# Performance work log

Measured on AMD Instinct MI355X. Metric: run time of the kernel, lower is better.

## Reference

```python
import jax, jax.numpy as jnp
import numpy as np
import math

D = 1024      # d_model
K = 64        # k_eigenstates
H = 4         # n_heads
KH = K // H   # eigenstates per head
MLP = 4 * D
B, T = 4, 4096


def setup_inputs() -> dict:
    key = jax.random.key(0)
    ks = jax.random.split(key, 16)
    rn = lambda k, shape, s: (jax.random.normal(k, shape, jnp.float32) * s)
    inp = {
        "x": rn(ks[0], (B, T, D), 1.0),
        "W_in": rn(ks[1], (2 * K, D), 1.0 / math.sqrt(D)),
        "log_decay": jax.random.uniform(ks[2], (K,), jnp.float32, -3.0, -0.1),
        "frequency": jnp.linspace(0.0, 2 * math.pi * (1 - 1.0 / K), K, dtype=jnp.float32),
        "W_sel": rn(ks[3], (2 * K, D), 0.01 / math.sqrt(D)),
        "b_sel": jnp.zeros((2 * K,), jnp.float32),
        "R": jnp.eye(KH, dtype=jnp.float32)[None] + 0.01 * rn(ks[4], (H, KH, KH), 1.0 / math.sqrt(KH)),
        "W_out": rn(ks[5], (D, 2 * K), 1.0 / math.sqrt(2 * K)),
        "W_g": rn(ks[6], (D, D), 1.0 / math.sqrt(D)),
        "b_g": jnp.full((D,), -2.0, jnp.float32),
        "g1": jnp.ones((D,), jnp.float32),
        "be1": jnp.zeros((D,), jnp.float32),
        "g2": jnp.ones((D,), jnp.float32),
        "be2": jnp.zeros((D,), jnp.float32),
        "W1": rn(ks[7], (MLP, D), 1.0 / math.sqrt(D)),
        "b1": jnp.zeros((MLP,), jnp.float32),
        "W2": rn(ks[8], (D, MLP), 1.0 / math.sqrt(MLP)),
        "b2": jnp.zeros((D,), jnp.float32),
    }
    return inp


def _ln(x, g, b):
    m = jnp.mean(x, axis=-1, keepdims=True)
    v = jnp.mean(jnp.square(x - m), axis=-1, keepdims=True)
    return (x - m) * jax.lax.rsqrt(v + 1e-5) * g + b


def _scan_combine(e1, e2):
    a1, b1 = e1
    a2, b2 = e2
    return a1 * a2, a2 * b1 + b2


def reference(x, W_in, log_decay, frequency, W_sel, b_sel, R, W_out, W_g, b_g,
              g1, be1, g2, be2, W1, b1, W2, b2):
    Bsz, Ts, Dm = x.shape
    residual = x
    x_norm = _ln(x, g1, be1)

    beta = x_norm @ W_in.T                      # [B,T,2K]
    beta_r, beta_i = jnp.split(beta, 2, axis=-1)

    delta = x_norm @ W_sel.T + b_sel            # selective modulation
    d_dec, d_fr = jnp.split(delta, 2, axis=-1)
    mag = jax.nn.sigmoid(log_decay + 0.1 * jnp.tanh(d_dec))   # [B,T,K]
    freq = frequency + 0.05 * jnp.tanh(d_fr)

    a = jax.lax.complex(mag * jnp.cos(freq), mag * jnp.sin(freq))  # lambda_t
    bc = jax.lax.complex(beta_r, beta_i)
    # inclusive prefix scan of c_t = a_t * c_{t-1} + b_t
    _, c = jax.lax.associative_scan(_scan_combine, (a, bc), axis=1)
    c_r, c_i = c.real, c.imag                   # [B,T,K]

    nH, Kh = R.shape[0], R.shape[1]
    c_r = jnp.einsum('hjk,bthk->bthj', R, c_r.reshape(Bsz, Ts, nH, Kh)).reshape(Bsz, Ts, -1)
    c_i = jnp.einsum('hjk,bthk->bthj', R, c_i.reshape(Bsz, Ts, nH, Kh)).reshape(Bsz, Ts, -1)

    h = jnp.concatenate([c_r, c_i], axis=-1) @ W_out.T
    gate = jax.nn.sigmoid(x_norm @ W_g.T + b_g)
    x = residual + gate * h

    x2 = _ln(x, g2, be2)
    x = x + (jax.nn.silu(x2 @ W1.T + b1) @ W2.T + b2)
    return x
```

## Files before the change

kernel.cpp:

```cpp
#include <hip/hip_runtime.h>
#include <math.h>

typedef __bf16 bf16_t;
typedef __attribute__((ext_vector_type(8))) __bf16 bf16x8;
typedef __attribute__((ext_vector_type(4))) float f32x4;

#define DMODEL 1024
#define NROWS  16384
#define SEQLEN 4096

static __device__ __forceinline__ float sigmoidf_(float v) { return 1.f / (1.f + __expf(-v)); }

#define GLOAD16(gsrc, ldst) __builtin_amdgcn_global_load_lds(                     \
    (const __attribute__((address_space(1))) void*)(gsrc),                        \
    (__attribute__((address_space(3))) void*)(ldst), 16, 0, 0)

__global__ __launch_bounds__(256) void ln_fused_kernel(const float* __restrict__ x,
                                                       const float* __restrict__ g,
                                                       const float* __restrict__ b,
                                                       bf16_t* __restrict__ out) {
  int row = blockIdx.x;
  int tid = threadIdx.x;
  const float4* xr = (const float4*)(x + (size_t)row * DMODEL);
  float4 v = xr[tid];
  float s  = v.x + v.y + v.z + v.w;
  float s2 = v.x*v.x + v.y*v.y + v.z*v.z + v.w*v.w;
  #pragma unroll
  for (int off = 32; off > 0; off >>= 1) {
    s  += __shfl_down(s, off);
    s2 += __shfl_down(s2, off);
  }
  __shared__ float sh[4], sh2[4];
  int lane = tid & 63, wid = tid >> 6;
  if (lane == 0) { sh[wid] = s; sh2[wid] = s2; }
  __syncthreads();
  s  = sh[0] + sh[1] + sh[2] + sh[3];
  s2 = sh2[0] + sh2[1] + sh2[2] + sh2[3];
  float m = s * (1.f / DMODEL);
  float var = fmaxf(s2 * (1.f / DMODEL) - m * m, 0.f);
  float rs = rsqrtf(var + 1e-5f);
  float4 gv = *(const float4*)&g[tid * 4];
  float4 bv = *(const float4*)&b[tid * 4];
  union { bf16_t h[4]; float2 f2; } u;
  u.h[0] = (bf16_t)((v.x - m) * rs * gv.x + bv.x);
  u.h[1] = (bf16_t)((v.y - m) * rs * gv.y + bv.y);
  u.h[2] = (bf16_t)((v.z - m) * rs * gv.z + bv.z);
  u.h[3] = (bf16_t)((v.w - m) * rs * gv.w + bv.w);
  *(float2*)&out[(size_t)row * DMODEL + tid * 4] = u.f2;
}

__global__ __launch_bounds__(256) void f32_to_bf16_kernel(const float* __restrict__ in,
                                                          bf16_t* __restrict__ out, int n) {
  int idx = (blockIdx.x * 256 + threadIdx.x) * 4;
  if (idx >= n) return;
  float4 v = *(const float4*)&in[idx];
  union { bf16_t h[4]; float2 f2; } u;
  u.h[0] = (bf16_t)v.x; u.h[1] = (bf16_t)v.y; u.h[2] = (bf16_t)v.z; u.h[3] = (bf16_t)v.w;
  *(float2*)&out[idx] = u.f2;
}

#define LOADA(d, mh)                                                              \
  { _Pragma("unroll")                                                             \
    for (int m_ = 0; m_ < 4; ++m_) {                                              \
      _Pragma("unroll")                                                           \
      for (int kk_ = 0; kk_ < 2; ++kk_)                                           \
        afrag[m_][kk_] = *(const bf16x8*)(ldsp + (d) * 32768 + (mh) * 16384 +     \
            (aRow + m_ * 16) * 128 + ((kk_ * 64 + q16) ^ swz));                   \
    } }

#define LOADB(d, nn)                                                              \
  { _Pragma("unroll")                                                             \
    for (int n2_ = 0; n2_ < 2; ++n2_) {                                           \
      _Pragma("unroll")                                                           \
      for (int kk_ = 0; kk_ < 2; ++kk_)                                           \
        bfrag[nn][n2_][kk_] = *(const bf16x8*)(ldsp + 65536 + (d) * 32768 +       \
            (nn) * 16384 + (bRow + n2_ * 16) * 128 + ((kk_ * 64 + q16) ^ swz));   \
    } }

#define MFMAQ(mh, nn)                                                             \
  { _Pragma("unroll")                                                             \
    for (int m_ = 0; m_ < 4; ++m_) {                                              \
      _Pragma("unroll")                                                           \
      for (int n2_ = 0; n2_ < 2; ++n2_) {                                         \
        acc[(mh)*4+m_][(nn)*2+n2_] = __builtin_amdgcn_mfma_f32_16x16x32_bf16(     \
            afrag[m_][0], bfrag[nn][n2_][0], acc[(mh)*4+m_][(nn)*2+n2_], 0,0,0);  \
        acc[(mh)*4+m_][(nn)*2+n2_] = __builtin_amdgcn_mfma_f32_16x16x32_bf16(     \
            afrag[m_][1], bfrag[nn][n2_][1], acc[(mh)*4+m_][(nn)*2+n2_], 0,0,0);  \
      }                                                                           \
    } }

#define PH_PRE()  __builtin_amdgcn_s_barrier();                                   \
                  asm volatile("s_waitcnt lgkmcnt(0)");                           \
                  __builtin_amdgcn_sched_barrier(0);                              \
                  __builtin_amdgcn_s_setprio(1)
#define PH_POST() __builtin_amdgcn_s_setprio(0);                                  \
                  __builtin_amdgcn_s_barrier()

template<int EPI>
__global__ __launch_bounds__(512, 2) void gemm256_kernel(
    const bf16_t* __restrict__ A, int lda,
    const bf16_t* __restrict__ B, int ldb, int K, int nx,
    const float* __restrict__ bias,
    const float* __restrict__ res,
    const float* __restrict__ aux,
    float* __restrict__ outf, bf16_t* __restrict__ outb, int ldout) {
  __shared__ __align__(128) char ldsp[131072];
  const int nwg = gridDim.x;
  const int bid = blockIdx.x;
  const int lid = (bid & 7) * (nwg >> 3) + (bid >> 3);
  const int n0 = (lid % nx) * 256;
  const int r0 = (lid / nx) * 256;

  const int tid = threadIdx.x;
  const int lane = tid & 63;
  const int w = tid >> 6;
  const int wr = w >> 2, wc = w & 3;
  const int fr = lane & 15;
  const int q16 = (lane >> 4) * 16;
  const int swz = (fr & 7) << 4;
  const int aRow = wr * 64 + fr;
  const int bRow = wc * 32 + fr;

  const size_t lda_b = (size_t)lda * 2;
  const size_t ldb_b = (size_t)ldb * 2;
  const char* Ab = (const char*)A;
  const char* Bb = (const char*)B;
  const int trow = tid >> 3;
  const int scolb = (((tid & 7) ^ (trow & 7)) << 4);

  auto stageA = [&](int d, int h, int kt) {
    const char* src = Ab + (size_t)(r0 + h * 64 + trow) * lda_b + kt * 128 + scolb;
    char* dst = ldsp + d * 32768 + h * 16384 + tid * 16;
    GLOAD16(src, dst);
    GLOAD16(src + 128 * lda_b, dst + 8192);
  };
  auto stageB = [&](int d, int g, int kt) {
    const int r1 = 64 + trow;
    const char* s0 = Bb + (size_t)(n0 + (trow >> 5) * 64 + g * 32 + (trow & 31)) * ldb_b + kt * 128 + scolb;
    const char* s1 = Bb + (size_t)(n0 + (r1 >> 5) * 64 + g * 32 + (r1 & 31)) * ldb_b + kt * 128 + scolb;
    char* dst = ldsp + 65536 + d * 32768 + g * 16384 + tid * 16;
    GLOAD16(s0, dst);
    GLOAD16(s1, dst + 8192);
  };

  f32x4 acc[8][4];
  #pragma unroll
  for (int m = 0; m < 8; ++m)
    #pragma unroll
    for (int n = 0; n < 4; ++n) acc[m][n] = (f32x4){0.f, 0.f, 0.f, 0.f};
  bf16x8 afrag[4][2];
  bf16x8 bfrag[2][2][2];

  const int nt = K >> 6;

  stageA(0, 0, 0); stageB(0, 0, 0); stageB(0, 1, 0); stageA(0, 1, 0);
  if (nt > 1) {
    stageA(1, 0, 1); stageB(1, 0, 1); stageB(1, 1, 1);
    asm volatile("s_waitcnt vmcnt(6)");
  } else {
    asm volatile("s_waitcnt vmcnt(0)");
  }
  __builtin_amdgcn_s_barrier();

  for (int t = 0; t < nt - 1; ++t) {
    const int d = t & 1, dn = d ^ 1;
    LOADA(d, 0) LOADB(d, 0)
    stageA(dn, 1, t + 1);
    PH_PRE(); MFMAQ(0, 0) PH_POST();
    LOADB(d, 1)
    if (t + 2 < nt) stageA(d, 0, t + 2);
    PH_PRE(); MFMAQ(0, 1) PH_POST();
    LOADA(d, 1)
    if (t + 2 < nt) stageB(d, 0, t + 2);
    PH_PRE(); MFMAQ(1, 0) PH_POST();
    if (t + 2 < nt) stageB(d, 1, t + 2);
    __builtin_amdgcn_s_barrier();
    __builtin_amdgcn_s_setprio(1);
    MFMAQ(1, 1)
    __builtin_amdgcn_s_setprio(0);
    if (t == nt - 2) { asm volatile("s_waitcnt vmcnt(0)"); }
    else             { asm volatile("s_waitcnt vmcnt(6)"); }
    __builtin_amdgcn_s_barrier();
  }
  {
    const int d = (nt - 1) & 1;
    LOADA(d, 0) LOADB(d, 0)
    asm volatile("s_waitcnt lgkmcnt(0)");
    __builtin_amdgcn_sched_barrier(0);
    MFMAQ(0, 0)
    LOADB(d, 1)
    asm volatile("s_waitcnt lgkmcnt(0)");
    __builtin_amdgcn_sched_barrier(0);
    MFMAQ(0, 1)
    LOADA(d, 1)
    asm volatile("s_waitcnt lgkmcnt(0)");
    __builtin_amdgcn_sched_barrier(0);
    MFMAQ(1, 0)
    MFMAQ(1, 1)
  }

  const int rbase = (lane >> 4) * 4;
  #pragma unroll
  for (int mf = 0; mf < 8; ++mf) {
    #pragma unroll
    for (int n = 0; n < 4; ++n) {
      int row = r0 + wr * 128 + mf * 16 + rbase;
      int col = n0 + wc * 64 + n * 16 + fr;
      f32x4 v = acc[mf][n];
      #pragma unroll
      for (int j = 0; j < 4; ++j) {
        int r = row + j;
        float val = v[j];
        if (EPI == 0) {
          outf[(size_t)r * ldout + col] = val;
        } else if (EPI == 1) {
          float t2 = val + bias[col];
          t2 = t2 * sigmoidf_(t2);
          outb[(size_t)r * ldout + col] = (bf16_t)t2;
        } else if (EPI == 2) {
          outf[(size_t)r * ldout + col] = res[(size_t)r * 1024 + col] + bias[col] + val;
        } else if (EPI == 3) {
          outf[(size_t)r * ldout + col] += val;
        } else {
          size_t idx = (size_t)r * 1024 + col;
          outf[idx] = res[idx] + sigmoidf_(val + bias[col]) * aux[idx];
        }
      }
    }
  }
}

template<int EPI>
__global__ __launch_bounds__(256) void gemm_bf16_kernel(
    const bf16_t* __restrict__ A, int lda,
    const bf16_t* __restrict__ B, int ldb, int K, int nx,
    float* __restrict__ outf, int ldout) {
  __shared__ __align__(16) bf16_t As[128 * 32];
  __shared__ __align__(16) bf16_t Bs[128 * 32];
  const int nwg = gridDim.x;
  const int bid = blockIdx.x;
  const int lid = (bid & 7) * (nwg >> 3) + (bid >> 3);
  const int n0 = (lid % nx) * 128;
  const int r0 = (lid / nx) * 128;

  const int tid = threadIdx.x;
  const int lane = tid & 63;
  const int w = tid >> 6;
  const int wr = w >> 1, wc = w & 1;
  const int srow0 = tid >> 2;
  const int srow1 = 64 + (tid >> 2);
  const int skk = (tid & 3) * 8;
  const int fr = lane & 15;
  const int ko = (lane >> 4) * 8;

  f32x4 acc[4][4];
  #pragma unroll
  for (int m = 0; m < 4; ++m)
    #pragma unroll
    for (int n = 0; n < 4; ++n) acc[m][n] = (f32x4){0.f, 0.f, 0.f, 0.f};

  for (int k0 = 0; k0 < K; k0 += 32) {
    GLOAD16(A + (size_t)(r0 + srow0) * lda + k0 + skk, (char*)As + w * 1024);
    GLOAD16(A + (size_t)(r0 + srow1) * lda + k0 + skk, (char*)As + 4096 + w * 1024);
    GLOAD16(B + (size_t)(n0 + srow0) * ldb + k0 + skk, (char*)Bs + w * 1024);
    GLOAD16(B + (size_t)(n0 + srow1) * ldb + k0 + skk, (char*)Bs + 4096 + w * 1024);
    __syncthreads();
    bf16x8 af[4], bfr[4];
    #pragma unroll
    for (int m = 0; m < 4; ++m)
      af[m] = *(const bf16x8*)&As[(wr * 64 + m * 16 + fr) * 32 + ko];
    #pragma unroll
    for (int n = 0; n < 4; ++n)
      bfr[n] = *(const bf16x8*)&Bs[(wc * 64 + n * 16 + fr) * 32 + ko];
    #pragma unroll
    for (int m = 0; m < 4; ++m)
      #pragma unroll
      for (int n = 0; n < 4; ++n)
        acc[m][n] = __builtin_amdgcn_mfma_f32_16x16x32_bf16(af[m], bfr[n], acc[m][n], 0, 0, 0);
    __syncthreads();
  }

  const int rbase = (lane >> 4) * 4;
  #pragma unroll
  for (int m = 0; m < 4; ++m) {
    #pragma unroll
    for (int n = 0; n < 4; ++n) {
      int row = r0 + wr * 64 + m * 16 + rbase;
      int col = n0 + wc * 64 + n * 16 + fr;
      f32x4 v = acc[m][n];
      #pragma unroll
      for (int j = 0; j < 4; ++j)
        outf[(size_t)(row + j) * ldout + col] = v[j];
    }
  }
}

__global__ __launch_bounds__(256) void ew_ab_kernel(
    const float* __restrict__ bd, const float* __restrict__ b_sel,
    const float* __restrict__ log_decay, const float* __restrict__ frequency,
    float* __restrict__ a_r, float* __restrict__ a_i,
    float* __restrict__ b_r, float* __restrict__ b_i) {
  __shared__ float T[32][257];
  int bb = blockIdx.x >> 7;
  int t0 = (blockIdx.x & 127) << 5;
  int tid = threadIdx.x;
  #pragma unroll
  for (int p = 0; p < 32; ++p) {
    int idx = tid + p * 256;
    int tt = idx >> 8, j = idx & 255;
    T[tt][j] = bd[((size_t)bb * 4096 + t0 + tt) * 256 + j];
  }
  __syncthreads();
  #pragma unroll
  for (int p = 0; p < 8; ++p) {
    int idx = tid + p * 256;
    int tt = idx & 31, k = idx >> 5;
    float br_ = T[tt][k];
    float bi_ = T[tt][64 + k];
    float dd = T[tt][128 + k] + b_sel[k];
    float df = T[tt][192 + k] + b_sel[64 + k];
    float mag = sigmoidf_(log_decay[k] + 0.1f * tanhf(dd));
    float fr = frequency[k] + 0.05f * tanhf(df);
    float ar_ = mag * cosf(fr), ai_ = mag * sinf(fr);
    size_t o = ((size_t)bb * 64 + k) * 4096 + t0 + tt;
    a_r[o] = ar_; a_i[o] = ai_; b_r[o] = br_; b_i[o] = bi_;
  }
}

__global__ __launch_bounds__(256) void scan_kernel(
    const float* __restrict__ a_r, const float* __restrict__ a_i,
    const float* b_r, const float* b_i,
    float* c_r, float* c_i) {
  int seq = blockIdx.x;
  size_t base = (size_t)seq * SEQLEN;
  int tid = threadIdx.x;
  int t0 = tid * 16;
  float Ar = 1.f, Ai = 0.f, Br = 0.f, Bi = 0.f;
  #pragma unroll
  for (int s = 0; s < 16; ++s) {
    size_t t = base + t0 + s;
    float ar = a_r[t], ai = a_i[t], br = b_r[t], bi = b_i[t];
    float nBr = ar * Br - ai * Bi + br;
    float nBi = ar * Bi + ai * Br + bi;
    Br = nBr; Bi = nBi;
    float nAr = ar * Ar - ai * Ai;
    float nAi = ar * Ai + ai * Ar;
    Ar = nAr; Ai = nAi;
  }
  __shared__ float sAr[256], sAi[256], sBr[256], sBi[256];
  sAr[tid] = Ar; sAi[tid] = Ai; sBr[tid] = Br; sBi[tid] = Bi;
  for (int off = 1; off < 256; off <<= 1) {
    __syncthreads();
    float pAr = 0.f, pAi = 0.f, pBr = 0.f, pBi = 0.f;
    if (tid >= off) { pAr = sAr[tid - off]; pAi = sAi[tid - off]; pBr = sBr[tid - off]; pBi = sBi[tid - off]; }
    __syncthreads();
    if (tid >= off) {
      float cAr = sAr[tid], cAi = sAi[tid], cBr = sBr[tid], cBi = sBi[tid];
      float nBr = cAr * pBr - cAi * pBi + cBr;
      float nBi = cAr * pBi + cAi * pBr + cBi;
      float nAr = cAr * pAr - cAi * pAi;
      float nAi = cAr * pAi + cAi * pAr;
      sAr[tid] = nAr; sAi[tid] = nAi; sBr[tid] = nBr; sBi[tid] = nBi;
    }
  }
  __syncthreads();
  float cr = (tid > 0) ? sBr[tid - 1] : 0.f;
  float ci = (tid > 0) ? sBi[tid - 1] : 0.f;
  #pragma unroll
  for (int s = 0; s < 16; ++s) {
    size_t t = base + t0 + s;
    float ar = a_r[t], ai = a_i[t], br = b_r[t], bi = b_i[t];
    float nr = ar * cr - ai * ci + br;
    float ni = ar * ci + ai * cr + bi;
    cr = nr; ci = ni;
    c_r[t] = cr; c_i[t] = ci;
  }
}

__global__ __launch_bounds__(256) void transpose_cc_kernel(
    const float* __restrict__ c_r, const float* __restrict__ c_i,
    bf16_t* __restrict__ cc) {
  __shared__ float Tr[64][65];
  __shared__ float Ti[64][65];
  int t0 = blockIdx.x * 64;
  int bb = blockIdx.y;
  int tid = threadIdx.x;
  int tt = tid & 63;
  int q = tid >> 6;
  #pragma unroll
  for (int p = 0; p < 16; ++p) {
    int k = p * 4 + q;
    size_t src = ((size_t)bb * 64 + k) * 4096 + t0 + tt;
    Tr[tt][k] = c_r[src];
    Ti[tt][k] = c_i[src];
  }
  __syncthreads();
  #pragma unroll
  for (int p = 0; p < 16; ++p) {
    int tt2 = p * 4 + q;
    int k = tid & 63;
    size_t row = (size_t)bb * 4096 + t0 + tt2;
    cc[row * 128 + k] = (bf16_t)Tr[tt2][k];
    cc[row * 128 + 64 + k] = (bf16_t)Ti[tt2][k];
  }
}

__global__ __launch_bounds__(256) void weff_kernel(const float* __restrict__ W_out,
                                                   const float* __restrict__ R,
                                                   bf16_t* __restrict__ Weff) {
  int idx = blockIdx.x * 256 + threadIdx.x;
  int d = idx >> 7, col = idx & 127;
  int k = col & 63, h = k >> 4, kk = k & 15;
  int off = (col < 64) ? 0 : 64;
  float s = 0.f;
  #pragma unroll
  for (int j = 0; j < 16; ++j)
    s += W_out[d * 128 + off + h * 16 + j] * R[h * 256 + j * 16 + kk];
  Weff[idx] = (bf16_t)s;
}

extern "C" void kernel_launch(void* const* d_in, const int* in_sizes, int n_in,
                              void* d_out, int out_size, void* d_ws, size_t ws_size,
                              hipStream_t stream) {
  (void)in_sizes; (void)n_in; (void)out_size; (void)ws_size;
  const float* x         = (const float*)d_in[0];
  const float* W_in      = (const float*)d_in[1];
  const float* log_decay = (const float*)d_in[2];
  const float* frequency = (const float*)d_in[3];
  const float* W_sel     = (const float*)d_in[4];
  const float* b_sel     = (const float*)d_in[5];
  const float* R         = (const float*)d_in[6];
  const float* W_out     = (const float*)d_in[7];
  const float* W_g       = (const float*)d_in[8];
  const float* b_g       = (const float*)d_in[9];
  const float* g1        = (const float*)d_in[10];
  const float* be1       = (const float*)d_in[11];
  const float* g2        = (const float*)d_in[12];
  const float* be2       = (const float*)d_in[13];
  const float* W1        = (const float*)d_in[14];
  const float* b1        = (const float*)d_in[15];
  const float* W2        = (const float*)d_in[16];
  const float* b2        = (const float*)d_in[17];
  float* out = (float*)d_out;
  float* ws  = (float*)d_ws;

  const size_t M1 = (size_t)1 << 20;
  float* bd   = ws;
  float* xmid = ws;
  float* a_r  = ws + 16 * M1;
  float* a_i  = ws + 20 * M1;
  float* b_rr = ws + 24 * M1;
  float* b_ii = ws + 28 * M1;
  float* hbuf = ws + 16 * M1;
  bf16_t* mid = (bf16_t*)(ws + 16 * M1);
  bf16_t* xn  = (bf16_t*)(ws + 32 * M1);
  bf16_t* cc  = (bf16_t*)(ws + 40 * M1);
  bf16_t* Wbd = (bf16_t*)(ws + 41 * M1);
  bf16_t* Wgb = (bf16_t*)(ws + 41 * M1 + (128 << 10));
  bf16_t* W1b = (bf16_t*)(ws + 41 * M1 + (640 << 10));
  bf16_t* W2b = (bf16_t*)(ws + 43 * M1 + (640 << 10));
  bf16_t* Wef = (bf16_t*)(ws + 45 * M1 + (640 << 10));

  dim3 blk(256);
  dim3 blk512(512);

  ln_fused_kernel<<<NROWS, blk, 0, stream>>>(x, g1, be1, xn);

  f32_to_bf16_kernel<<<128, blk, 0, stream>>>(W_in, Wbd, 128 * 1024);
  f32_to_bf16_kernel<<<128, blk, 0, stream>>>(W_sel, Wbd + 128 * 1024, 128 * 1024);
  f32_to_bf16_kernel<<<1024, blk, 0, stream>>>(W_g, Wgb, 1024 * 1024);
  f32_to_bf16_kernel<<<4096, blk, 0, stream>>>(W1, W1b, 4 * 1024 * 1024);
  f32_to_bf16_kernel<<<4096, blk, 0, stream>>>(W2, W2b, 4 * 1024 * 1024);
  weff_kernel<<<512, blk, 0, stream>>>(W_out, R, Wef);

  gemm_bf16_kernel<0><<<256, blk, 0, stream>>>(xn, 1024, Wbd, 1024, 1024, 2, bd, 256);

  ew_ab_kernel<<<512, blk, 0, stream>>>(bd, b_sel, log_decay, frequency, a_r, a_i, b_rr, b_ii);
  scan_kernel<<<256, blk, 0, stream>>>(a_r, a_i, b_rr, b_ii, b_rr, b_ii);
  transpose_cc_kernel<<<dim3(64, 4), blk, 0, stream>>>(b_rr, b_ii, cc);

  gemm256_kernel<0><<<256, blk512, 0, stream>>>(
      cc, 128, Wef, 128, 128, 4, nullptr, nullptr, nullptr, hbuf, nullptr, 1024);

  gemm256_kernel<4><<<256, blk512, 0, stream>>>(
      xn, 1024, Wgb, 1024, 1024, 4, b_g, x, hbuf, xmid, nullptr, 1024);

  ln_fused_kernel<<<NROWS, blk, 0, stream>>>(xmid, g2, be2, xn);

  for (int h = 0; h < 2; ++h) {
    gemm256_kernel<1><<<512, blk512, 0, stream>>>(
        xn, 1024, W1b + (size_t)h * 2048 * 1024, 1024, 1024, 8,
        b1 + h * 2048, nullptr, nullptr, nullptr, mid, 2048);
    if (h == 0) {
      gemm256_kernel<2><<<256, blk512, 0, stream>>>(
          mid, 2048, W2b, 4096, 2048, 4,
          b2, xmid, nullptr, out, nullptr, 1024);
    } else {
      gemm256_kernel<3><<<256, blk512, 0, stream>>>(
          mid, 2048, W2b + 2048, 4096, 2048, 4,
          nullptr, nullptr, nullptr, out, nullptr, 1024);
    }
  }
}
```

Baseline: 527.0 us.

## Unroll GEMM mainloop by two K-tiles with inline-asm LDS reads and static buffers

Reads LDS fragments with inline ds_read_b128 using precomputed base pointers and immediate offsets, which drops per-load address arithmetic. Unrolls the main loop two K-tiles at a time so the double-buffer index is a compile-time constant. Reorders the global->LDS staging inside the phases and adjusts the vmcnt waits. The code now assumes an even tile count with at least two tiles, and the hand-written waitcnt/barrier choreography risks races if a count is wrong.

```diff
diff --git a/kernel.cpp b/kernel.cpp
--- a/kernel.cpp
+++ b/kernel.cpp
@@ -59,23 +59,25 @@
   *(float2*)&out[idx] = u.f2;
 }
 
-#define LOADA(d, mh)                                                              \
-  { _Pragma("unroll")                                                             \
-    for (int m_ = 0; m_ < 4; ++m_) {                                              \
-      _Pragma("unroll")                                                           \
-      for (int kk_ = 0; kk_ < 2; ++kk_)                                           \
-        afrag[m_][kk_] = *(const bf16x8*)(ldsp + (d) * 32768 + (mh) * 16384 +     \
-            (aRow + m_ * 16) * 128 + ((kk_ * 64 + q16) ^ swz));                   \
-    } }
-
-#define LOADB(d, nn)                                                              \
-  { _Pragma("unroll")                                                             \
-    for (int n2_ = 0; n2_ < 2; ++n2_) {                                           \
-      _Pragma("unroll")                                                           \
-      for (int kk_ = 0; kk_ < 2; ++kk_)                                           \
-        bfrag[nn][n2_][kk_] = *(const bf16x8*)(ldsp + 65536 + (d) * 32768 +       \
-            (nn) * 16384 + (bRow + n2_ * 16) * 128 + ((kk_ * 64 + q16) ^ swz));   \
-    } }
+
+#define DSR128(dst, ptr, IMM) \
+  asm volatile("ds_read_b128 %0, %1 offset:%2" : "=v"(dst) : "v"(ptr), "n"(IMM))
+
+#define LOADA(d_, mh_)                                                     \
+  DSR128(afrag[0][0], pA0, (d_)*32768+(mh_)*16384+0*2048);                 \
+  DSR128(afrag[0][1], pA1, (d_)*32768+(mh_)*16384+0*2048);                 \
+  DSR128(afrag[1][0], pA0, (d_)*32768+(mh_)*16384+1*2048);                 \
+  DSR128(afrag[1][1], pA1, (d_)*32768+(mh_)*16384+1*2048);                 \
+  DSR128(afrag[2][0], pA0, (d_)*32768+(mh_)*16384+2*2048);                 \
+  DSR128(afrag[2][1], pA1, (d_)*32768+(mh_)*16384+2*2048);                 \
+  DSR128(afrag[3][0], pA0, (d_)*32768+(mh_)*16384+3*2048);                 \
+  DSR128(afrag[3][1], pA1, (d_)*32768+(mh_)*16384+3*2048);
+
+#define LOADB(d_, nn_)                                                     \
+  DSR128(bfrag[nn_][0][0], pB0, (d_)*32768+(nn_)*16384+0*2048);            \
+  DSR128(bfrag[nn_][0][1], pB1, (d_)*32768+(nn_)*16384+0*2048);            \
+  DSR128(bfrag[nn_][1][0], pB0, (d_)*32768+(nn_)*16384+1*2048);            \
+  DSR128(bfrag[nn_][1][1], pB1, (d_)*32768+(nn_)*16384+1*2048);
 
 #define MFMAQ(mh, nn)                                                             \
   { _Pragma("unroll")                                                             \
@@ -104,7 +106,7 @@
     const float* __restrict__ res,
     const float* __restrict__ aux,
     float* __restrict__ outf, bf16_t* __restrict__ outb, int ldout) {
-  __shared__ __align__(128) char ldsp[131072];
+  __shared__ __align__(1024) char ldsp[131072];
   const int nwg = gridDim.x;
   const int bid = blockIdx.x;
   const int lid = (bid & 7) * (nwg >> 3) + (bid >> 3);
@@ -120,6 +122,13 @@
   const int swz = (fr & 7) << 4;
   const int aRow = wr * 64 + fr;
   const int bRow = wc * 32 + fr;
+
+  typedef __attribute__((address_space(3))) char lds_char;
+  lds_char* lb = (lds_char*)ldsp;
+  lds_char* pA0 = lb + aRow * 128 + (q16 ^ swz);
+  lds_char* pA1 = lb + aRow * 128 + ((64 + q16) ^ swz);
+  lds_char* pB0 = lb + 65536 + bRow * 128 + (q16 ^ swz);
+  lds_char* pB1 = lb + 65536 + bRow * 128 + ((64 + q16) ^ swz);
 
   const size_t lda_b = (size_t)lda * 2;
   const size_t ldb_b = (size_t)ldb * 2;
@@ -152,52 +161,62 @@
   bf16x8 bfrag[2][2][2];
 
   const int nt = K >> 6;
+  const int np = nt >> 1;
 
   stageA(0, 0, 0); stageB(0, 0, 0); stageB(0, 1, 0); stageA(0, 1, 0);
-  if (nt > 1) {
-    stageA(1, 0, 1); stageB(1, 0, 1); stageB(1, 1, 1);
+  stageA(1, 0, 1); stageB(1, 0, 1); stageB(1, 1, 1); stageA(1, 1, 1);
+  asm volatile("s_waitcnt vmcnt(8)");
+  __builtin_amdgcn_s_barrier();
+
+  for (int i = 0; i < np - 1; ++i) {
+    const int t2 = 2 * i + 2, t3 = 2 * i + 3;
+    LOADA(0, 0) LOADB(0, 0)
+    PH_PRE(); MFMAQ(0, 0) PH_POST();
+    stageA(0, 0, t2);
+    LOADB(0, 1)
+    PH_PRE(); MFMAQ(0, 1) PH_POST();
+    stageB(0, 0, t2);
+    LOADA(0, 1)
+    PH_PRE(); MFMAQ(1, 0) PH_POST();
+    stageB(0, 1, t2);
+    PH_PRE(); MFMAQ(1, 1)
+    __builtin_amdgcn_s_setprio(0);
     asm volatile("s_waitcnt vmcnt(6)");
-  } else {
-    asm volatile("s_waitcnt vmcnt(0)");
-  }
+    __builtin_amdgcn_s_barrier();
+    stageA(0, 1, t2);
+    LOADA(1, 0) LOADB(1, 0)
+    PH_PRE(); MFMAQ(0, 0) PH_POST();
+    stageA(1, 0, t3);
+    LOADB(1, 1)
+    PH_PRE(); MFMAQ(0, 1) PH_POST();
+    stageB(1, 0, t3);
+    LOADA(1, 1)
+    PH_PRE(); MFMAQ(1, 0) PH_POST();
+    stageB(1, 1, t3); stageA(1, 1, t3);
+    PH_PRE(); MFMAQ(1, 1)
+    __builtin_amdgcn_s_setprio(0);
+    asm volatile("s_waitcnt vmcnt(8)");
+    __builtin_amdgcn_s_barrier();
+  }
+
+  LOADA(0, 0) LOADB(0, 0)
+  PH_PRE(); MFMAQ(0, 0) PH_POST();
+  LOADB(0, 1)
+  PH_PRE(); MFMAQ(0, 1) PH_POST();
+  LOADA(0, 1)
+  PH_PRE(); MFMAQ(1, 0) PH_POST();
+  PH_PRE(); MFMAQ(1, 1)
+  __builtin_amdgcn_s_setprio(0);
+  asm volatile("s_waitcnt vmcnt(0)");
   __builtin_amdgcn_s_barrier();
-
-  for (int t = 0; t < nt - 1; ++t) {
-    const int d = t & 1, dn = d ^ 1;
-    LOADA(d, 0) LOADB(d, 0)
-    stageA(dn, 1, t + 1);
-    PH_PRE(); MFMAQ(0, 0) PH_POST();
-    LOADB(d, 1)
-    if (t + 2 < nt) stageA(d, 0, t + 2);
-    PH_PRE(); MFMAQ(0, 1) PH_POST();
-    LOADA(d, 1)
-    if (t + 2 < nt) stageB(d, 0, t + 2);
-    PH_PRE(); MFMAQ(1, 0) PH_POST();
-    if (t + 2 < nt) stageB(d, 1, t + 2);
-    __builtin_amdgcn_s_barrier();
-    __builtin_amdgcn_s_setprio(1);
-    MFMAQ(1, 1)
-    __builtin_amdgcn_s_setprio(0);
-    if (t == nt - 2) { asm volatile("s_waitcnt vmcnt(0)"); }
-    else             { asm volatile("s_waitcnt vmcnt(6)"); }
-    __builtin_amdgcn_s_barrier();
-  }
-  {
-    const int d = (nt - 1) & 1;
-    LOADA(d, 0) LOADB(d, 0)
-    asm volatile("s_waitcnt lgkmcnt(0)");
-    __builtin_amdgcn_sched_barrier(0);
-    MFMAQ(0, 0)
-    LOADB(d, 1)
-    asm volatile("s_waitcnt lgkmcnt(0)");
-    __builtin_amdgcn_sched_barrier(0);
-    MFMAQ(0, 1)
-    LOADA(d, 1)
-    asm volatile("s_waitcnt lgkmcnt(0)");
-    __builtin_amdgcn_sched_barrier(0);
-    MFMAQ(1, 0)
-    MFMAQ(1, 1)
-  }
+  LOADA(1, 0) LOADB(1, 0)
+  PH_PRE(); MFMAQ(0, 0) PH_POST();
+  LOADB(1, 1)
+  PH_PRE(); MFMAQ(0, 1) PH_POST();
+  LOADA(1, 1)
+  PH_PRE(); MFMAQ(1, 0) PH_POST();
+  PH_PRE(); MFMAQ(1, 1)
+  __builtin_amdgcn_s_setprio(0);
 
   const int rbase = (lane >> 4) * 4;
   #pragma unroll
```

After: 533.3 us. Within noise of the previous version (+1.2%).
